# Performance work log

Measured on AMD Instinct MI355X. Metric: run time of the kernel, lower is better.

Reference implementation:

```python
import jax, jax.numpy as jnp
import numpy as np

N = 50000   # n_nodes (== input_dim, featureless identity features)
E = 800000  # edges per support (avg degree 16)
D = 200     # embed_dim (hardcoded in GIN)
C = 10      # num_classes


def setup_inputs() -> dict:
    key = jax.random.key(0)
    ks = jax.random.split(key, 8)
    x = jnp.zeros((N, 1), jnp.float32)  # unused: layer 0 is featureless
    rows0 = jax.random.randint(ks[0], (E,), 0, N, dtype=jnp.int32)
    cols0 = jax.random.randint(ks[1], (E,), 0, N, dtype=jnp.int32)
    vals0 = jax.random.uniform(ks[2], (E,), jnp.float32)
    rows1 = jax.random.randint(ks[3], (E,), 0, N, dtype=jnp.int32)
    cols1 = jax.random.randint(ks[4], (E,), 0, N, dtype=jnp.int32)
    vals1 = jax.random.uniform(ks[5], (E,), jnp.float32)
    W0 = jax.random.normal(ks[6], (N, D), jnp.float32) * 0.02
    W1 = jax.random.normal(ks[7], (D, C), jnp.float32) * 0.05
    eps0 = jnp.zeros((1,), jnp.float32)  # train_eps init (~1e-4 in repo)
    eps1 = jnp.zeros((1,), jnp.float32)
    return dict(x=x, rows0=rows0, cols0=cols0, vals0=vals0,
                rows1=rows1, cols1=cols1, vals1=vals1,
                W0=W0, W1=W1, eps0=eps0, eps1=eps1)


def reference(x, rows0, cols0, vals0, rows1, cols1, vals1, W0, W1, eps0, eps1):
    # sparse A @ X via gather + segment-sum (A in COO: rows, cols, vals)
    def spmm(r, c, v, X):
        return jax.ops.segment_sum(v[:, None] * X[c], r, num_segments=N)

    # Layer 0 (featureless, num_mlp_layers==1):
    #   AX = sum_i A_i ; out = AX @ W0 + 0.1*(1+eps0)*W0
    h0 = spmm(rows0, cols0, vals0, W0) + spmm(rows1, cols1, vals1, W0) \
         + 0.1 * (1.0 + eps0[0]) * W0
    h = jax.nn.relu(h0)  # [N, D]

    # Layer 1 (with features): out = (sum_i A_i @ h + 0.1*(1+eps1)*h) @ W1
    ax = spmm(rows0, cols0, vals0, h) + spmm(rows1, cols1, vals1, h)
    out = (ax + 0.1 * (1.0 + eps1[0]) * h) @ W1  # [N, C]
    return out
```

## Files before the change

### kernel.cpp

```cpp
#include <hip/hip_runtime.h>

#define N_NODES 50000
#define E_EDGES 800000
#define E2      (2 * E_EDGES)
#define D_DIM   200
#define C_CLS   10
#define NB_BUCKET 196
#define BATCH     4096
#define NB_SCATTER ((E2 + BATCH - 1) / BATCH)
#define NB_CONV    ((N_NODES * D_DIM / 4 + 255) / 256)
#define CAP       12288

static __device__ __forceinline__ unsigned f2bf(float f) {
    unsigned u = __float_as_uint(f);
    return (u + 0x7FFFu + ((u >> 16) & 1u)) >> 16;
}
static __device__ __forceinline__ float bf_lo(unsigned u) {
    return __uint_as_float(u << 16);
}
static __device__ __forceinline__ float bf_hi(unsigned u) {
    return __uint_as_float(u & 0xFFFF0000u);
}

__global__ __launch_bounds__(256) void convert_scatter_kernel(
        const float* __restrict__ W0, unsigned short* __restrict__ W0h,
        const int* __restrict__ rows0, const int* __restrict__ cols0,
        const float* __restrict__ vals0,
        const int* __restrict__ rows1, const int* __restrict__ cols1,
        const float* __restrict__ vals1,
        int* __restrict__ bcur,
        int2* __restrict__ stage) {
    __shared__ int cntL[NB_BUCKET];
    __shared__ int baseL[NB_BUCKET];
    __shared__ int offL[NB_BUCKET];
    __shared__ int2 recL[BATCH];

    if (blockIdx.x >= NB_SCATTER) {
        int i = ((blockIdx.x - NB_SCATTER) * 256 + threadIdx.x) * 4;
        if (i < N_NODES * D_DIM) {
            float4 f = *(const float4*)(W0 + i);
            uint2 p;
            p.x = f2bf(f.x) | (f2bf(f.y) << 16);
            p.y = f2bf(f.z) | (f2bf(f.w) << 16);
            *(uint2*)(W0h + i) = p;
        }
        return;
    }

    const int tid = threadIdx.x;
    const int e0 = blockIdx.x * BATCH;

    for (int b = tid; b < NB_BUCKET; b += 256) cntL[b] = 0;
    __syncthreads();

#pragma unroll
    for (int k = 0; k < BATCH / 256; ++k) {
        int idx = k * 256 + tid;
        int e = e0 + idx;
        if (e < E2) {
            int r, c;
            float v;
            if (e < E_EDGES) {
                r = rows0[e]; c = cols0[e]; v = vals0[e];
            } else {
                int e1 = e - E_EDGES;
                r = rows1[e1]; c = cols1[e1]; v = vals1[e1];
            }
            recL[idx] = make_int2((int)((unsigned)r | ((unsigned)c << 16)),
                                  __float_as_int(v));
            atomicAdd(&cntL[r >> 8], 1);
        }
    }
    __syncthreads();

    for (int b = tid; b < NB_BUCKET; b += 256) {
        int c = cntL[b];
        baseL[b] = (c > 0) ? atomicAdd(&bcur[b], c) : 0;
        offL[b] = 0;
    }
    __syncthreads();

#pragma unroll
    for (int k = 0; k < BATCH / 256; ++k) {
        int idx = k * 256 + tid;
        int e = e0 + idx;
        if (e < E2) {
            int2 rec = recL[idx];
            int b = (int)(((unsigned)rec.x & 0xFFFFu) >> 8);
            int pos = baseL[b] + atomicAdd(&offL[b], 1);
            stage[(size_t)b * CAP + pos] = rec;
        }
    }
}

__global__ __launch_bounds__(256) void build_csr_kernel(
        const int* __restrict__ bcur,
        const int2* __restrict__ stage,
        int* __restrict__ ticket,
        int2* __restrict__ rowseg,
        unsigned* __restrict__ cv4) {
    __shared__ int hist[256];
    __shared__ int lcur[256];
    __shared__ int ws4[4];
    __shared__ int sbase;
    const int b = blockIdx.x;
    const int tid = threadIdx.x;
    const int lane = tid & 63;
    const int w = tid >> 6;
    hist[tid] = 0;
    __syncthreads();

    const int n = bcur[b];
    const int2* __restrict__ sp = stage + (size_t)b * CAP;
    for (int i = tid; i < n; i += 256)
        atomicAdd(&hist[(unsigned)sp[i].x & 255u], 1);
    __syncthreads();

    int v = hist[tid];
    const int orig = v;
#pragma unroll
    for (int off = 1; off < 64; off <<= 1) {
        int t = __shfl_up(v, off, 64);
        if (lane >= off) v += t;
    }
    if (lane == 63) ws4[w] = v;
    __syncthreads();
    if (tid == 0) {
        int s = 0;
#pragma unroll
        for (int k = 0; k < 4; ++k) { int t = ws4[k]; ws4[k] = s; s += t; }
    }
    __syncthreads();
    v += ws4[w];

    if (tid == 255) sbase = atomicAdd(ticket, v);
    __syncthreads();

    const int start = sbase + v - orig;
    const int row = (b << 8) + tid;
    if (row < N_NODES) rowseg[row] = make_int2(start, orig);
    lcur[tid] = start;
    __syncthreads();

    for (int i = tid; i < n; i += 256) {
        int2 rec = sp[i];
        unsigned u = (unsigned)rec.x;
        int pos = atomicAdd(&lcur[u & 255u], 1);
        cv4[pos] = (u & 0xFFFF0000u) | f2bf(__int_as_float(rec.y));
    }
}

__global__ __launch_bounds__(256) void spmm_layer0_fused_kernel(
        const int2* __restrict__ rowseg,
        const unsigned* __restrict__ cv4,
        const unsigned short* __restrict__ W0h,
        const float* __restrict__ W1,
        const float* __restrict__ eps0,
        float* __restrict__ g) {
    __shared__ float W1s[D_DIM * C_CLS];
    for (int i = threadIdx.x; i < D_DIM * C_CLS; i += blockDim.x) W1s[i] = W1[i];
    __syncthreads();

    const int lane = threadIdx.x & 63;
    const int n = __builtin_amdgcn_readfirstlane(blockIdx.x * 4 + (threadIdx.x >> 6));
    if (n >= N_NODES) return;
    const float s0 = 0.1f * (1.0f + eps0[0]);
    const bool act = (lane < 50);
    const uint2* __restrict__ F = (const uint2*)W0h;

    const int2 seg = rowseg[n];
    const int beg  = seg.x;
    const int endp = seg.x + seg.y;
    float a0 = 0.f, a1 = 0.f, a2 = 0.f, a3 = 0.f;

    int e = beg;
    for (; e + 8 <= endp; e += 8) {
        unsigned w0 = cv4[e],     w1 = cv4[e + 1], w2 = cv4[e + 2], w3 = cv4[e + 3];
        unsigned w4 = cv4[e + 4], w5 = cv4[e + 5], w6 = cv4[e + 6], w7 = cv4[e + 7];
        if (act) {
            uint2 u0 = F[(size_t)(w0 >> 16) * 50 + lane];
            uint2 u1 = F[(size_t)(w1 >> 16) * 50 + lane];
            uint2 u2 = F[(size_t)(w2 >> 16) * 50 + lane];
            uint2 u3 = F[(size_t)(w3 >> 16) * 50 + lane];
            uint2 u4 = F[(size_t)(w4 >> 16) * 50 + lane];
            uint2 u5 = F[(size_t)(w5 >> 16) * 50 + lane];
            uint2 u6 = F[(size_t)(w6 >> 16) * 50 + lane];
            uint2 u7 = F[(size_t)(w7 >> 16) * 50 + lane];
            float v0 = __uint_as_float(w0 << 16), v1 = __uint_as_float(w1 << 16);
            float v2 = __uint_as_float(w2 << 16), v3 = __uint_as_float(w3 << 16);
            float v4 = __uint_as_float(w4 << 16), v5 = __uint_as_float(w5 << 16);
            float v6 = __uint_as_float(w6 << 16), v7 = __uint_as_float(w7 << 16);
            a0 += v0 * bf_lo(u0.x) + v1 * bf_lo(u1.x) + v2 * bf_lo(u2.x) + v3 * bf_lo(u3.x)
                + v4 * bf_lo(u4.x) + v5 * bf_lo(u5.x) + v6 * bf_lo(u6.x) + v7 * bf_lo(u7.x);
            a1 += v0 * bf_hi(u0.x) + v1 * bf_hi(u1.x) + v2 * bf_hi(u2.x) + v3 * bf_hi(u3.x)
                + v4 * bf_hi(u4.x) + v5 * bf_hi(u5.x) + v6 * bf_hi(u6.x) + v7 * bf_hi(u7.x);
            a2 += v0 * bf_lo(u0.y) + v1 * bf_lo(u1.y) + v2 * bf_lo(u2.y) + v3 * bf_lo(u3.y)
                + v4 * bf_lo(u4.y) + v5 * bf_lo(u5.y) + v6 * bf_lo(u6.y) + v7 * bf_lo(u7.y);
            a3 += v0 * bf_hi(u0.y) + v1 * bf_hi(u1.y) + v2 * bf_hi(u2.y) + v3 * bf_hi(u3.y)
                + v4 * bf_hi(u4.y) + v5 * bf_hi(u5.y) + v6 * bf_hi(u6.y) + v7 * bf_hi(u7.y);
        }
    }
    for (; e + 4 <= endp; e += 4) {
        unsigned w0 = cv4[e], w1 = cv4[e + 1], w2 = cv4[e + 2], w3 = cv4[e + 3];
        if (act) {
            uint2 u0 = F[(size_t)(w0 >> 16) * 50 + lane];
            uint2 u1 = F[(size_t)(w1 >> 16) * 50 + lane];
            uint2 u2 = F[(size_t)(w2 >> 16) * 50 + lane];
            uint2 u3 = F[(size_t)(w3 >> 16) * 50 + lane];
            float v0 = __uint_as_float(w0 << 16), v1 = __uint_as_float(w1 << 16);
            float v2 = __uint_as_float(w2 << 16), v3 = __uint_as_float(w3 << 16);
            a0 += v0 * bf_lo(u0.x) + v1 * bf_lo(u1.x) + v2 * bf_lo(u2.x) + v3 * bf_lo(u3.x);
            a1 += v0 * bf_hi(u0.x) + v1 * bf_hi(u1.x) + v2 * bf_hi(u2.x) + v3 * bf_hi(u3.x);
            a2 += v0 * bf_lo(u0.y) + v1 * bf_lo(u1.y) + v2 * bf_lo(u2.y) + v3 * bf_lo(u3.y);
            a3 += v0 * bf_hi(u0.y) + v1 * bf_hi(u1.y) + v2 * bf_hi(u2.y) + v3 * bf_hi(u3.y);
        }
    }
    for (; e < endp; ++e) {
        unsigned w = cv4[e];
        if (act) {
            uint2 u = F[(size_t)(w >> 16) * 50 + lane];
            float v = __uint_as_float(w << 16);
            a0 += v * bf_lo(u.x);
            a1 += v * bf_hi(u.x);
            a2 += v * bf_lo(u.y);
            a3 += v * bf_hi(u.y);
        }
    }

    float o[C_CLS];
#pragma unroll
    for (int k = 0; k < C_CLS; ++k) o[k] = 0.f;

    if (act) {
        uint2 w = F[(size_t)n * 50 + lane];
        a0 = fmaxf(a0 + s0 * bf_lo(w.x), 0.f);
        a1 = fmaxf(a1 + s0 * bf_hi(w.x), 0.f);
        a2 = fmaxf(a2 + s0 * bf_lo(w.y), 0.f);
        a3 = fmaxf(a3 + s0 * bf_hi(w.y), 0.f);
        const int d = lane * 4;
#pragma unroll
        for (int k = 0; k < C_CLS; ++k) {
            o[k] = a0 * W1s[(d + 0) * C_CLS + k]
                 + a1 * W1s[(d + 1) * C_CLS + k]
                 + a2 * W1s[(d + 2) * C_CLS + k]
                 + a3 * W1s[(d + 3) * C_CLS + k];
        }
    }

#pragma unroll
    for (int k = 0; k < C_CLS; ++k) {
        for (int off = 32; off > 0; off >>= 1)
            o[k] += __shfl_xor(o[k], off, 64);
    }

    if (lane == 0) {
        float* gp = g + (size_t)n * C_CLS;
#pragma unroll
        for (int k = 0; k < C_CLS; ++k) gp[k] = o[k];
    }
}

__global__ __launch_bounds__(256) void spmm_layer1_light_kernel(
        const int2* __restrict__ rowseg,
        const unsigned* __restrict__ cv4,
        const float* __restrict__ g,
        const float* __restrict__ eps1,
        float* __restrict__ out) {
    const int lane = threadIdx.x & 63;
    const int n = __builtin_amdgcn_readfirstlane(blockIdx.x * 4 + (threadIdx.x >> 6));
    if (n >= N_NODES) return;
    const int grp = lane / 10;
    const int d   = lane - grp * 10;
    const float s1 = 0.1f * (1.0f + eps1[0]);

    const int2 seg = rowseg[n];
    const int beg  = seg.x;
    const int endp = seg.x + seg.y;
    float acc = 0.f;

    for (int base = beg; base < endp; base += 12) {
        if (grp < 6) {
            int ea = base + grp;
            int eb = base + 6 + grp;
            unsigned pa = (ea < endp) ? cv4[ea] : 0u;
            unsigned pb = (eb < endp) ? cv4[eb] : 0u;
            if (ea < endp)
                acc += __uint_as_float(pa << 16) * g[(size_t)(pa >> 16) * C_CLS + d];
            if (eb < endp)
                acc += __uint_as_float(pb << 16) * g[(size_t)(pb >> 16) * C_CLS + d];
        }
    }

    float t;
    t = __shfl(acc, lane + 10, 64); if (lane < 50) acc += t;
    t = __shfl(acc, lane + 20, 64); if (lane < 30) acc += t;
    t = __shfl(acc, lane + 40, 64); if (lane < 10) acc += t;

    if (lane < 10) {
        out[(size_t)n * C_CLS + d] = acc + s1 * g[(size_t)n * C_CLS + d];
    }
}

extern "C" void kernel_launch(void* const* d_in, const int* in_sizes, int n_in,
                              void* d_out, int out_size, void* d_ws, size_t ws_size,
                              hipStream_t stream) {
    const int*   rows0 = (const int*)d_in[1];
    const int*   cols0 = (const int*)d_in[2];
    const float* vals0 = (const float*)d_in[3];
    const int*   rows1 = (const int*)d_in[4];
    const int*   cols1 = (const int*)d_in[5];
    const float* vals1 = (const float*)d_in[6];
    const float* W0    = (const float*)d_in[7];
    const float* W1    = (const float*)d_in[8];
    const float* eps0  = (const float*)d_in[9];
    const float* eps1  = (const float*)d_in[10];
    float* out = (float*)d_out;

    char* ws = (char*)d_ws;
    size_t off = 0;
    auto alloc = [&](size_t bytes) {
        void* p = ws + off;
        off += (bytes + 255) & ~(size_t)255;
        return p;
    };
    unsigned short* W0h = (unsigned short*)alloc((size_t)N_NODES * D_DIM * 2);
    float* g      = (float*)alloc((size_t)N_NODES * C_CLS * 4);
    int2* rowseg  = (int2*)alloc((size_t)N_NODES * 8);
    int* bcur     = (int*)alloc((size_t)(NB_BUCKET + 1) * 4);
    unsigned* cv4 = (unsigned*)alloc((size_t)E2 * 4);
    int2* stage   = (int2*)alloc((size_t)NB_BUCKET * CAP * 8);
    int* ticket   = bcur + NB_BUCKET;
    (void)ws_size;

    hipMemsetAsync(bcur, 0, (size_t)(NB_BUCKET + 1) * 4, stream);
    convert_scatter_kernel<<<NB_SCATTER + NB_CONV, 256, 0, stream>>>(
        W0, W0h, rows0, cols0, vals0, rows1, cols1, vals1, bcur, stage);
    build_csr_kernel<<<NB_BUCKET, 256, 0, stream>>>(bcur, stage, ticket, rowseg, cv4);

    const int spmm_grid = (N_NODES + 3) / 4;
    spmm_layer0_fused_kernel<<<spmm_grid, 256, 0, stream>>>(
        rowseg, cv4, W0h, W1, eps0, g);
    spmm_layer1_light_kernel<<<spmm_grid, 256, 0, stream>>>(
        rowseg, cv4, g, eps1, out);
}
```

Before: 272.2 us.

## Sort CSR edges by column window and process eight rows per wave for gather locality

The CSR build now bins each row's edges into 13 column windows (col>>12) so that within a row the edges are grouped by source-column range. The layer-0 SpMM assigns eight rows per wavefront and walks all eight rows window by window, so concurrent gathers of W0 rows stay within a narrower address range and reuse cache better. W1 is also transposed in shared memory so the final projection can use float4 reads. The cost is serial one-edge-at-a-time inner loops with data-dependent breaks, no unrolled batched loads, more registers, and fewer waves in flight.

```diff
diff --git a/kernel.cpp b/kernel.cpp
--- a/kernel.cpp
+++ b/kernel.cpp
@@ -10,6 +10,9 @@
 #define NB_SCATTER ((E2 + BATCH - 1) / BATCH)
 #define NB_CONV    ((N_NODES * D_DIM / 4 + 255) / 256)
 #define CAP       12288
+#define NWIN      13
+#define RPW       8
+#define NB_L0     ((N_NODES + 4 * RPW - 1) / (4 * RPW))
 
 static __device__ __forceinline__ unsigned f2bf(float f) {
     unsigned u = __float_as_uint(f);
@@ -99,25 +102,30 @@
         int* __restrict__ ticket,
         int2* __restrict__ rowseg,
         unsigned* __restrict__ cv4) {
-    __shared__ int hist[256];
-    __shared__ int lcur[256];
+    __shared__ int hist[256 * NWIN];
     __shared__ int ws4[4];
     __shared__ int sbase;
     const int b = blockIdx.x;
     const int tid = threadIdx.x;
     const int lane = tid & 63;
     const int w = tid >> 6;
-    hist[tid] = 0;
+
+    for (int i = tid; i < 256 * NWIN; i += 256) hist[i] = 0;
     __syncthreads();
 
     const int n = bcur[b];
     const int2* __restrict__ sp = stage + (size_t)b * CAP;
-    for (int i = tid; i < n; i += 256)
-        atomicAdd(&hist[(unsigned)sp[i].x & 255u], 1);
-    __syncthreads();
-
-    int v = hist[tid];
-    const int orig = v;
+    for (int i = tid; i < n; i += 256) {
+        unsigned u = (unsigned)sp[i].x;
+        atomicAdd(&hist[(u & 255u) * NWIN + (u >> 28)], 1);
+    }
+    __syncthreads();
+
+    int rowtot = 0;
+#pragma unroll
+    for (int k = 0; k < NWIN; ++k) rowtot += hist[tid * NWIN + k];
+
+    int v = rowtot;
 #pragma unroll
     for (int off = 1; off < 64; off <<= 1) {
         int t = __shfl_up(v, off, 64);
@@ -136,127 +144,112 @@
     if (tid == 255) sbase = atomicAdd(ticket, v);
     __syncthreads();
 
-    const int start = sbase + v - orig;
+    const int start = sbase + v - rowtot;
     const int row = (b << 8) + tid;
-    if (row < N_NODES) rowseg[row] = make_int2(start, orig);
-    lcur[tid] = start;
+    if (row < N_NODES) rowseg[row] = make_int2(start, rowtot);
+
+    int c = start;
+#pragma unroll
+    for (int k = 0; k < NWIN; ++k) {
+        int t = hist[tid * NWIN + k];
+        hist[tid * NWIN + k] = c;
+        c += t;
+    }
     __syncthreads();
 
     for (int i = tid; i < n; i += 256) {
         int2 rec = sp[i];
         unsigned u = (unsigned)rec.x;
-        int pos = atomicAdd(&lcur[u & 255u], 1);
+        int pos = atomicAdd(&hist[(u & 255u) * NWIN + (u >> 28)], 1);
         cv4[pos] = (u & 0xFFFF0000u) | f2bf(__int_as_float(rec.y));
     }
 }
 
-__global__ __launch_bounds__(256) void spmm_layer0_fused_kernel(
+__global__ __launch_bounds__(256, 6) void spmm_layer0_fused_kernel(
         const int2* __restrict__ rowseg,
         const unsigned* __restrict__ cv4,
         const unsigned short* __restrict__ W0h,
         const float* __restrict__ W1,
         const float* __restrict__ eps0,
         float* __restrict__ g) {
-    __shared__ float W1s[D_DIM * C_CLS];
-    for (int i = threadIdx.x; i < D_DIM * C_CLS; i += blockDim.x) W1s[i] = W1[i];
+    __shared__ __align__(16) float W1Ts[C_CLS * D_DIM];
+    for (int i = threadIdx.x; i < C_CLS * D_DIM; i += 256) {
+        int k = i / D_DIM, d = i - k * D_DIM;
+        W1Ts[i] = W1[d * C_CLS + k];
+    }
     __syncthreads();
 
     const int lane = threadIdx.x & 63;
-    const int n = __builtin_amdgcn_readfirstlane(blockIdx.x * 4 + (threadIdx.x >> 6));
-    if (n >= N_NODES) return;
+    const int wid = blockIdx.x * 4 + (threadIdx.x >> 6);
+    const int n0 = wid * RPW;
+    if (n0 >= N_NODES) return;
     const float s0 = 0.1f * (1.0f + eps0[0]);
     const bool act = (lane < 50);
     const uint2* __restrict__ F = (const uint2*)W0h;
 
-    const int2 seg = rowseg[n];
-    const int beg  = seg.x;
-    const int endp = seg.x + seg.y;
-    float a0 = 0.f, a1 = 0.f, a2 = 0.f, a3 = 0.f;
-
-    int e = beg;
-    for (; e + 8 <= endp; e += 8) {
-        unsigned w0 = cv4[e],     w1 = cv4[e + 1], w2 = cv4[e + 2], w3 = cv4[e + 3];
-        unsigned w4 = cv4[e + 4], w5 = cv4[e + 5], w6 = cv4[e + 6], w7 = cv4[e + 7];
+    int cur[RPW], end_[RPW];
+#pragma unroll
+    for (int j = 0; j < RPW; ++j) {
+        int2 s = rowseg[n0 + j];
+        cur[j] = s.x;
+        end_[j] = s.x + s.y;
+    }
+    float a[RPW][4];
+#pragma unroll
+    for (int j = 0; j < RPW; ++j) { a[j][0] = a[j][1] = a[j][2] = a[j][3] = 0.f; }
+
+    for (int w = 0; w < NWIN; ++w) {
+        const unsigned wt = (unsigned)w;
+#pragma unroll
+        for (int j = 0; j < RPW; ++j) {
+            int e = cur[j];
+            const int ep = end_[j];
+            while (e < ep) {
+                unsigned u = cv4[e];
+                if ((u >> 28) != wt) break;
+                if (act) {
+                    uint2 q = F[(size_t)(u >> 16) * 50 + lane];
+                    float v = __uint_as_float(u << 16);
+                    a[j][0] += v * bf_lo(q.x);
+                    a[j][1] += v * bf_hi(q.x);
+                    a[j][2] += v * bf_lo(q.y);
+                    a[j][3] += v * bf_hi(q.y);
+                }
+                ++e;
+            }
+            cur[j] = e;
+        }
+    }
+
+    const float4* __restrict__ W1T4 = (const float4*)W1Ts;
+#pragma unroll
+    for (int j = 0; j < RPW; ++j) {
+        const int n = n0 + j;
+        float o[C_CLS];
+#pragma unroll
+        for (int k = 0; k < C_CLS; ++k) o[k] = 0.f;
         if (act) {
-            uint2 u0 = F[(size_t)(w0 >> 16) * 50 + lane];
-            uint2 u1 = F[(size_t)(w1 >> 16) * 50 + lane];
-            uint2 u2 = F[(size_t)(w2 >> 16) * 50 + lane];
-            uint2 u3 = F[(size_t)(w3 >> 16) * 50 + lane];
-            uint2 u4 = F[(size_t)(w4 >> 16) * 50 + lane];
-            uint2 u5 = F[(size_t)(w5 >> 16) * 50 + lane];
-            uint2 u6 = F[(size_t)(w6 >> 16) * 50 + lane];
-            uint2 u7 = F[(size_t)(w7 >> 16) * 50 + lane];
-            float v0 = __uint_as_float(w0 << 16), v1 = __uint_as_float(w1 << 16);
-            float v2 = __uint_as_float(w2 << 16), v3 = __uint_as_float(w3 << 16);
-            float v4 = __uint_as_float(w4 << 16), v5 = __uint_as_float(w5 << 16);
-            float v6 = __uint_as_float(w6 << 16), v7 = __uint_as_float(w7 << 16);
-            a0 += v0 * bf_lo(u0.x) + v1 * bf_lo(u1.x) + v2 * bf_lo(u2.x) + v3 * bf_lo(u3.x)
-                + v4 * bf_lo(u4.x) + v5 * bf_lo(u5.x) + v6 * bf_lo(u6.x) + v7 * bf_lo(u7.x);
-            a1 += v0 * bf_hi(u0.x) + v1 * bf_hi(u1.x) + v2 * bf_hi(u2.x) + v3 * bf_hi(u3.x)
-                + v4 * bf_hi(u4.x) + v5 * bf_hi(u5.x) + v6 * bf_hi(u6.x) + v7 * bf_hi(u7.x);
-            a2 += v0 * bf_lo(u0.y) + v1 * bf_lo(u1.y) + v2 * bf_lo(u2.y) + v3 * bf_lo(u3.y)
-                + v4 * bf_lo(u4.y) + v5 * bf_lo(u5.y) + v6 * bf_lo(u6.y) + v7 * bf_lo(u7.y);
-            a3 += v0 * bf_hi(u0.y) + v1 * bf_hi(u1.y) + v2 * bf_hi(u2.y) + v3 * bf_hi(u3.y)
-                + v4 * bf_hi(u4.y) + v5 * bf_hi(u5.y) + v6 * bf_hi(u6.y) + v7 * bf_hi(u7.y);
-        }
-    }
-    for (; e + 4 <= endp; e += 4) {
-        unsigned w0 = cv4[e], w1 = cv4[e + 1], w2 = cv4[e + 2], w3 = cv4[e + 3];
-        if (act) {
-            uint2 u0 = F[(size_t)(w0 >> 16) * 50 + lane];
-            uint2 u1 = F[(size_t)(w1 >> 16) * 50 + lane];
-            uint2 u2 = F[(size_t)(w2 >> 16) * 50 + lane];
-            uint2 u3 = F[(size_t)(w3 >> 16) * 50 + lane];
-            float v0 = __uint_as_float(w0 << 16), v1 = __uint_as_float(w1 << 16);
-            float v2 = __uint_as_float(w2 << 16), v3 = __uint_as_float(w3 << 16);
-            a0 += v0 * bf_lo(u0.x) + v1 * bf_lo(u1.x) + v2 * bf_lo(u2.x) + v3 * bf_lo(u3.x);
-            a1 += v0 * bf_hi(u0.x) + v1 * bf_hi(u1.x) + v2 * bf_hi(u2.x) + v3 * bf_hi(u3.x);
-            a2 += v0 * bf_lo(u0.y) + v1 * bf_lo(u1.y) + v2 * bf_lo(u2.y) + v3 * bf_lo(u3.y);
-            a3 += v0 * bf_hi(u0.y) + v1 * bf_hi(u1.y) + v2 * bf_hi(u2.y) + v3 * bf_hi(u3.y);
-        }
-    }
-    for (; e < endp; ++e) {
-        unsigned w = cv4[e];
-        if (act) {
-            uint2 u = F[(size_t)(w >> 16) * 50 + lane];
-            float v = __uint_as_float(w << 16);
-            a0 += v * bf_lo(u.x);
-            a1 += v * bf_hi(u.x);
-            a2 += v * bf_lo(u.y);
-            a3 += v * bf_hi(u.y);
-        }
-    }
-
-    float o[C_CLS];
-#pragma unroll
-    for (int k = 0; k < C_CLS; ++k) o[k] = 0.f;
-
-    if (act) {
-        uint2 w = F[(size_t)n * 50 + lane];
-        a0 = fmaxf(a0 + s0 * bf_lo(w.x), 0.f);
-        a1 = fmaxf(a1 + s0 * bf_hi(w.x), 0.f);
-        a2 = fmaxf(a2 + s0 * bf_lo(w.y), 0.f);
-        a3 = fmaxf(a3 + s0 * bf_hi(w.y), 0.f);
-        const int d = lane * 4;
+            uint2 wsv = F[(size_t)n * 50 + lane];
+            float a0 = fmaxf(a[j][0] + s0 * bf_lo(wsv.x), 0.f);
+            float a1 = fmaxf(a[j][1] + s0 * bf_hi(wsv.x), 0.f);
+            float a2 = fmaxf(a[j][2] + s0 * bf_lo(wsv.y), 0.f);
+            float a3 = fmaxf(a[j][3] + s0 * bf_hi(wsv.y), 0.f);
+#pragma unroll
+            for (int k = 0; k < C_CLS; ++k) {
+                float4 wv = W1T4[k * 50 + lane];
+                o[k] = a0 * wv.x + a1 * wv.y + a2 * wv.z + a3 * wv.w;
+            }
+        }
 #pragma unroll
         for (int k = 0; k < C_CLS; ++k) {
-            o[k] = a0 * W1s[(d + 0) * C_CLS + k]
-                 + a1 * W1s[(d + 1) * C_CLS + k]
-                 + a2 * W1s[(d + 2) * C_CLS + k]
-                 + a3 * W1s[(d + 3) * C_CLS + k];
-        }
-    }
-
-#pragma unroll
-    for (int k = 0; k < C_CLS; ++k) {
-        for (int off = 32; off > 0; off >>= 1)
-            o[k] += __shfl_xor(o[k], off, 64);
-    }
-
-    if (lane == 0) {
-        float* gp = g + (size_t)n * C_CLS;
-#pragma unroll
-        for (int k = 0; k < C_CLS; ++k) gp[k] = o[k];
+            for (int off = 32; off > 0; off >>= 1)
+                o[k] += __shfl_xor(o[k], off, 64);
+        }
+        if (lane == 0) {
+            float* gp = g + (size_t)n * C_CLS;
+#pragma unroll
+            for (int k = 0; k < C_CLS; ++k) gp[k] = o[k];
+        }
     }
 }
 
@@ -337,9 +330,9 @@
         W0, W0h, rows0, cols0, vals0, rows1, cols1, vals1, bcur, stage);
     build_csr_kernel<<<NB_BUCKET, 256, 0, stream>>>(bcur, stage, ticket, rowseg, cv4);
 
-    const int spmm_grid = (N_NODES + 3) / 4;
-    spmm_layer0_fused_kernel<<<spmm_grid, 256, 0, stream>>>(
+    spmm_layer0_fused_kernel<<<NB_L0, 256, 0, stream>>>(
         rowseg, cv4, W0h, W1, eps0, g);
-    spmm_layer1_light_kernel<<<spmm_grid, 256, 0, stream>>>(
+    const int spmm1_grid = (N_NODES + 3) / 4;
+    spmm_layer1_light_kernel<<<spmm1_grid, 256, 0, stream>>>(
         rowseg, cv4, g, eps1, out);
 }
```

Result: slower. 547.8 us (+101.2%).

## Drop LDS edge staging, widen CSR build blocks, transpose W1 in LDS

Applied to the files above, without the earlier changes.

The scatter kernel no longer buffers a 32 KB record array in LDS. It reads rows once to count buckets, then re-reads rows, cols and vals to emit records, which should raise occupancy at the cost of re-reading the row indices. The CSR build kernel moves from 256 to 1024 threads per bucket block so each of the 196 blocks has more parallelism, with the scan extended to 16 waves. Layer-0 stores W1 transposed in LDS so each class weight fetch is one float4 read instead of four strided scalar reads.

```diff
diff --git a/kernel.cpp b/kernel.cpp
--- a/kernel.cpp
+++ b/kernel.cpp
@@ -33,7 +33,6 @@
     __shared__ int cntL[NB_BUCKET];
     __shared__ int baseL[NB_BUCKET];
     __shared__ int offL[NB_BUCKET];
-    __shared__ int2 recL[BATCH];
 
     if (blockIdx.x >= NB_SCATTER) {
         int i = ((blockIdx.x - NB_SCATTER) * 256 + threadIdx.x) * 4;
@@ -55,8 +54,24 @@
 
 #pragma unroll
     for (int k = 0; k < BATCH / 256; ++k) {
-        int idx = k * 256 + tid;
-        int e = e0 + idx;
+        int e = e0 + k * 256 + tid;
+        if (e < E2) {
+            int r = (e < E_EDGES) ? rows0[e] : rows1[e - E_EDGES];
+            atomicAdd(&cntL[r >> 8], 1);
+        }
+    }
+    __syncthreads();
+
+    for (int b = tid; b < NB_BUCKET; b += 256) {
+        int c = cntL[b];
+        baseL[b] = (c > 0) ? atomicAdd(&bcur[b], c) : 0;
+        offL[b] = 0;
+    }
+    __syncthreads();
+
+#pragma unroll
+    for (int k = 0; k < BATCH / 256; ++k) {
+        int e = e0 + k * 256 + tid;
         if (e < E2) {
             int r, c;
             float v;
@@ -66,34 +81,16 @@
                 int e1 = e - E_EDGES;
                 r = rows1[e1]; c = cols1[e1]; v = vals1[e1];
             }
-            recL[idx] = make_int2((int)((unsigned)r | ((unsigned)c << 16)),
-                                  __float_as_int(v));
-            atomicAdd(&cntL[r >> 8], 1);
-        }
-    }
-    __syncthreads();
-
-    for (int b = tid; b < NB_BUCKET; b += 256) {
-        int c = cntL[b];
-        baseL[b] = (c > 0) ? atomicAdd(&bcur[b], c) : 0;
-        offL[b] = 0;
-    }
-    __syncthreads();
-
-#pragma unroll
-    for (int k = 0; k < BATCH / 256; ++k) {
-        int idx = k * 256 + tid;
-        int e = e0 + idx;
-        if (e < E2) {
-            int2 rec = recL[idx];
-            int b = (int)(((unsigned)rec.x & 0xFFFFu) >> 8);
+            int b = r >> 8;
             int pos = baseL[b] + atomicAdd(&offL[b], 1);
-            stage[(size_t)b * CAP + pos] = rec;
-        }
-    }
-}
-
-__global__ __launch_bounds__(256) void build_csr_kernel(
+            stage[(size_t)b * CAP + pos] =
+                make_int2((int)((unsigned)r | ((unsigned)c << 16)),
+                          __float_as_int(v));
+        }
+    }
+}
+
+__global__ __launch_bounds__(1024) void build_csr_kernel(
         const int* __restrict__ bcur,
         const int2* __restrict__ stage,
         int* __restrict__ ticket,
@@ -101,48 +98,51 @@
         unsigned* __restrict__ cv4) {
     __shared__ int hist[256];
     __shared__ int lcur[256];
-    __shared__ int ws4[4];
+    __shared__ int ws16[16];
     __shared__ int sbase;
     const int b = blockIdx.x;
     const int tid = threadIdx.x;
     const int lane = tid & 63;
     const int w = tid >> 6;
-    hist[tid] = 0;
+
+    if (tid < 256) hist[tid] = 0;
     __syncthreads();
 
     const int n = bcur[b];
     const int2* __restrict__ sp = stage + (size_t)b * CAP;
-    for (int i = tid; i < n; i += 256)
+    for (int i = tid; i < n; i += 1024)
         atomicAdd(&hist[(unsigned)sp[i].x & 255u], 1);
     __syncthreads();
 
-    int v = hist[tid];
-    const int orig = v;
+    const int cnt = (tid < 256) ? hist[tid] : 0;
+    int v = cnt;
 #pragma unroll
     for (int off = 1; off < 64; off <<= 1) {
         int t = __shfl_up(v, off, 64);
         if (lane >= off) v += t;
     }
-    if (lane == 63) ws4[w] = v;
+    if (lane == 63) ws16[w] = v;
     __syncthreads();
     if (tid == 0) {
         int s = 0;
 #pragma unroll
-        for (int k = 0; k < 4; ++k) { int t = ws4[k]; ws4[k] = s; s += t; }
-    }
-    __syncthreads();
-    v += ws4[w];
-
-    if (tid == 255) sbase = atomicAdd(ticket, v);
-    __syncthreads();
-
-    const int start = sbase + v - orig;
+        for (int k = 0; k < 16; ++k) { int t = ws16[k]; ws16[k] = s; s += t; }
+    }
+    __syncthreads();
+    v += ws16[w];
+
+    if (tid == 1023) sbase = atomicAdd(ticket, v);
+    __syncthreads();
+
+    const int start = sbase + v - cnt;
     const int row = (b << 8) + tid;
-    if (row < N_NODES) rowseg[row] = make_int2(start, orig);
-    lcur[tid] = start;
-    __syncthreads();
-
-    for (int i = tid; i < n; i += 256) {
+    if (tid < 256) {
+        if (row < N_NODES) rowseg[row] = make_int2(start, cnt);
+        lcur[tid] = start;
+    }
+    __syncthreads();
+
+    for (int i = tid; i < n; i += 1024) {
         int2 rec = sp[i];
         unsigned u = (unsigned)rec.x;
         int pos = atomicAdd(&lcur[u & 255u], 1);
@@ -157,8 +157,11 @@
         const float* __restrict__ W1,
         const float* __restrict__ eps0,
         float* __restrict__ g) {
-    __shared__ float W1s[D_DIM * C_CLS];
-    for (int i = threadIdx.x; i < D_DIM * C_CLS; i += blockDim.x) W1s[i] = W1[i];
+    __shared__ __align__(16) float W1Ts[C_CLS * D_DIM];
+    for (int i = threadIdx.x; i < C_CLS * D_DIM; i += 256) {
+        int k = i / D_DIM, d = i - k * D_DIM;
+        W1Ts[i] = W1[d * C_CLS + k];
+    }
     __syncthreads();
 
     const int lane = threadIdx.x & 63;
@@ -231,19 +234,17 @@
 #pragma unroll
     for (int k = 0; k < C_CLS; ++k) o[k] = 0.f;
 
+    const float4* __restrict__ W1T4 = (const float4*)W1Ts;
     if (act) {
         uint2 w = F[(size_t)n * 50 + lane];
         a0 = fmaxf(a0 + s0 * bf_lo(w.x), 0.f);
         a1 = fmaxf(a1 + s0 * bf_hi(w.x), 0.f);
         a2 = fmaxf(a2 + s0 * bf_lo(w.y), 0.f);
         a3 = fmaxf(a3 + s0 * bf_hi(w.y), 0.f);
-        const int d = lane * 4;
 #pragma unroll
         for (int k = 0; k < C_CLS; ++k) {
-            o[k] = a0 * W1s[(d + 0) * C_CLS + k]
-                 + a1 * W1s[(d + 1) * C_CLS + k]
-                 + a2 * W1s[(d + 2) * C_CLS + k]
-                 + a3 * W1s[(d + 3) * C_CLS + k];
+            float4 wv = W1T4[k * 50 + lane];
+            o[k] = a0 * wv.x + a1 * wv.y + a2 * wv.z + a3 * wv.w;
         }
     }
 
@@ -335,7 +336,7 @@
     hipMemsetAsync(bcur, 0, (size_t)(NB_BUCKET + 1) * 4, stream);
     convert_scatter_kernel<<<NB_SCATTER + NB_CONV, 256, 0, stream>>>(
         W0, W0h, rows0, cols0, vals0, rows1, cols1, vals1, bcur, stage);
-    build_csr_kernel<<<NB_BUCKET, 256, 0, stream>>>(bcur, stage, ticket, rowseg, cv4);
+    build_csr_kernel<<<NB_BUCKET, 1024, 0, stream>>>(bcur, stage, ticket, rowseg, cv4);
 
     const int spmm_grid = (N_NODES + 3) / 4;
     spmm_layer0_fused_kernel<<<spmm_grid, 256, 0, stream>>>(
```

Result: no change. 273.1 us (+0.3%).
